# Performance work log

Hardware: AMD Instinct MI355X
Metric: run time of the kernel (lower is better)

The kernel has to match this reference:

```python
import jax, jax.numpy as jnp
import numpy as np


def setup_inputs() -> dict:
    key = jax.random.key(0)
    k1, k2 = jax.random.split(key)
    x = jax.random.normal(k1, (16, 8192, 128), dtype=jnp.float32)
    embed = jax.random.normal(k2, (1024, 128), dtype=jnp.float32)
    return {"x": x, "embed": embed}


def reference(x, embed):
    # preprocess: flatten leading dims -> (N, d)
    shape = x.shape
    xf = x.reshape(-1, shape[-1])  # (N, d)
    # quantize: negative squared Euclidean distance, argmax over codebook
    dist = (2.0 * (xf @ embed.T)
            - jnp.sum(xf * xf, axis=1, keepdims=True)
            - jnp.sum(embed * embed, axis=1)[None, :])
    embed_ind = jnp.argmax(dist, axis=-1)  # (N,)
    # postprocess indices back to input leading shape
    embed_ind = embed_ind.reshape(shape[:-1])
    # dequantize: embedding lookup
    quantize = embed[embed_ind]  # (..., d)
    return embed_ind, quantize
```

## Files before the change

kernel.cpp:

```cpp
#include <hip/hip_runtime.h>
#include <math.h>


typedef __attribute__((ext_vector_type(8)))  short short8_t;
typedef __attribute__((ext_vector_type(16))) float floatx16;

constexpr int D        = 128;
constexpr int KCODES   = 1024;
constexpr int NTILES   = 32;
constexpr int ROWS_BLK = 128;
constexpr float TAU    = 0.015f;

constexpr size_t WS_NCSQ = 0;
constexpr size_t WS_EHI  = 4096;
constexpr size_t WS_ELO  = WS_EHI + 262144;
constexpr size_t WS_EMBT = WS_ELO + 262144;

__device__ inline unsigned short bf16_rne(float v, float* back) {
    unsigned u = __float_as_uint(v);
    unsigned r = (u + 0x7FFFu + ((u >> 16) & 1u)) >> 16;
    *back = __uint_as_float(r << 16);
    return (unsigned short)r;
}

__global__ __launch_bounds__(256)
void ecb_prep(const float* __restrict__ embed, float* __restrict__ ncsq,
              unsigned short* __restrict__ ehi, unsigned short* __restrict__ elo,
              float* __restrict__ embT) {
    const int tid = threadIdx.x;
    const int cc = tid & 15;
    const int nl = tid >> 4;
    const int n  = blockIdx.x * 16 + nl;
    const int t = n >> 5, nn = n & 31;
    const float* src = embed + (size_t)n * D + cc * 8;
    float4 a = *(const float4*)src;
    float4 b = *(const float4*)(src + 4);
    float vv[8] = {a.x, a.y, a.z, a.w, b.x, b.y, b.z, b.w};
    float ss = 0.f;
    unsigned short hq[8], lq[8];
#pragma unroll
    for (int j = 0; j < 8; ++j) {
        ss = fmaf(vv[j], vv[j], ss);
        float hb, db;
        hq[j] = bf16_rne(vv[j], &hb);
        lq[j] = bf16_rne(vv[j] - hb, &db);
    }
    uint4 ph, pl;
    ph.x = (unsigned)hq[0] | ((unsigned)hq[1] << 16);
    ph.y = (unsigned)hq[2] | ((unsigned)hq[3] << 16);
    ph.z = (unsigned)hq[4] | ((unsigned)hq[5] << 16);
    ph.w = (unsigned)hq[6] | ((unsigned)hq[7] << 16);
    pl.x = (unsigned)lq[0] | ((unsigned)lq[1] << 16);
    pl.y = (unsigned)lq[2] | ((unsigned)lq[3] << 16);
    pl.z = (unsigned)lq[4] | ((unsigned)lq[5] << 16);
    pl.w = (unsigned)lq[6] | ((unsigned)lq[7] << 16);
    size_t dst = ((size_t)(t * 8 + (cc >> 1)) * 64 + (size_t)((cc & 1) * 32 + nn)) * 8;
    *(uint4*)(ehi + dst) = ph;
    *(uint4*)(elo + dst) = pl;
#pragma unroll
    for (int j = 0; j < 8; ++j) embT[(size_t)(cc * 8 + j) * KCODES + n] = vv[j];
#pragma unroll
    for (int m = 1; m < 16; m <<= 1) ss += __shfl_xor(ss, m, 64);
    if (cc == 0) ncsq[n] = -ss;
}

__global__ __launch_bounds__(256, 2)
void ecb_main(const float* __restrict__ x,
              const unsigned short* __restrict__ ehi, const unsigned short* __restrict__ elo,
              const float* __restrict__ ncsq, const float* __restrict__ embed,
              const float* __restrict__ embT,
              float* __restrict__ out_idx, float* __restrict__ out_q) {
    __shared__ int   sidx[ROWS_BLK];
    __shared__ unsigned char llist[ROWS_BLK];
    __shared__ unsigned lcount;
    __shared__ float xs[D];
    __shared__ float bv[256];
    __shared__ int   bi[256];

    const int tid  = threadIdx.x;
    const int lane = tid & 63, wave = tid >> 6;
    const int col  = lane & 31, h = lane >> 5;
    const long rowblk = (long)blockIdx.x * ROWS_BLK;
    const int  roww   = wave * 32;

    if (tid == 0) lcount = 0u;

    short8_t ah[8], al[8];
    {
        const float* xr = x + (rowblk + roww + col) * (long)D + h * 8;
#pragma unroll
        for (int c = 0; c < 8; ++c) {
            float4 a  = *(const float4*)(xr + c * 16);
            float4 b  = *(const float4*)(xr + c * 16 + 4);
            float vv[8] = {a.x, a.y, a.z, a.w, b.x, b.y, b.z, b.w};
            short8_t fh, fl;
#pragma unroll
            for (int j = 0; j < 8; ++j) {
                float v2x = vv[j] + vv[j];
                float hb, db;
                fh[j] = (short)bf16_rne(v2x, &hb);
                fl[j] = (short)bf16_rne(v2x - hb, &db);
            }
            ah[c] = fh;
            al[c] = fl;
        }
    }

    float v1[16], v2[16];
#pragma unroll
    for (int j = 0; j < 16; ++j) { v1[j] = -INFINITY; v2[j] = -INFINITY; }

    const short8_t* Bh = (const short8_t*)ehi + lane;
    const short8_t* Bl = (const short8_t*)elo + lane;

    __syncthreads();

#pragma unroll 1
    for (int t = 0; t < NTILES; ++t) {
        const float negcs = ncsq[t * 32 + col];
        short8_t bh[8], bl[8];
#pragma unroll
        for (int s = 0; s < 8; ++s) {
            bh[s] = Bh[(size_t)(t * 8 + s) * 64];
            bl[s] = Bl[(size_t)(t * 8 + s) * 64];
        }
        floatx16 accA, accB;
#pragma unroll
        for (int i = 0; i < 16; ++i) { accA[i] = negcs; accB[i] = 0.f; }
#pragma unroll
        for (int s = 0; s < 8; ++s) {
            accA = __builtin_amdgcn_mfma_f32_32x32x16_bf16(ah[s], bh[s], accA, 0, 0, 0);
            accB = __builtin_amdgcn_mfma_f32_32x32x16_bf16(al[s], bh[s], accB, 0, 0, 0);
            accB = __builtin_amdgcn_mfma_f32_32x32x16_bf16(ah[s], bl[s], accB, 0, 0, 0);
        }
#pragma unroll
        for (int j = 0; j < 16; ++j) {
            float sc = accA[j] + accB[j];
            unsigned u = (__float_as_uint(sc) & ~31u) | (unsigned)t;
            float cand = __uint_as_float(u);
            float mn = fminf(v1[j], cand);
            v1[j] = fmaxf(v1[j], cand);
            v2[j] = fmaxf(v2[j], mn);
        }
        __builtin_amdgcn_s_barrier();
    }

#pragma unroll
    for (int j = 0; j < 16; ++j) {
        float a1 = v1[j], a2 = v2[j];
        int   c1 = (int)((__float_as_uint(a1) & 31u) << 5) | col;
#pragma unroll
        for (int m = 1; m < 32; m <<= 1) {
            float o1 = __shfl_xor(a1, m, 64);
            int   oc = __shfl_xor(c1, m, 64);
            float o2 = __shfl_xor(a2, m, 64);
            float lo = fminf(a1, o1);
            if (o1 > a1) { a1 = o1; c1 = oc; }
            a2 = fmaxf(fmaxf(a2, o2), lo);
        }
        if (col == j) {
            int row_local = roww + (j & 3) + 8 * (j >> 2) + 4 * h;
            sidx[row_local] = c1;
            out_idx[rowblk + row_local] = (float)c1;
            if (a1 - a2 < TAU) {
                unsigned p = atomicAdd(&lcount, 1u);
                llist[p] = (unsigned char)row_local;
            }
        }
    }
    __syncthreads();

    for (int i = tid; i < ROWS_BLK * 32; i += 256) {
        int r = i >> 5, q = i & 31;
        int code = sidx[r];
        float4 ev = *(const float4*)(embed + (size_t)code * D + q * 4);
        *(float4*)(out_q + (rowblk + r) * (long)D + q * 4) = ev;
    }
    __syncthreads();

    const unsigned nf = lcount;
    const float4* eT = (const float4*)embT;
    for (unsigned f = 0; f < nf; ++f) {
        const int rl  = llist[f];
        const long row = rowblk + rl;
        if (tid < 32) *(float4*)&xs[tid * 4] = *(const float4*)(x + row * D + tid * 4);
        __syncthreads();
        float4 dot = {0.f, 0.f, 0.f, 0.f};
#pragma unroll 8
        for (int k = 0; k < D; ++k) {
            float xv = xs[k];
            float4 e = eT[(size_t)k * 256 + tid];
            dot.x = fmaf(xv, e.x, dot.x);
            dot.y = fmaf(xv, e.y, dot.y);
            dot.z = fmaf(xv, e.z, dot.z);
            dot.w = fmaf(xv, e.w, dot.w);
        }
        const int c0 = tid * 4;
        float scs[4] = {fmaf(2.f, dot.x, ncsq[c0]),
                        fmaf(2.f, dot.y, ncsq[c0 + 1]),
                        fmaf(2.f, dot.z, ncsq[c0 + 2]),
                        fmaf(2.f, dot.w, ncsq[c0 + 3])};
        float best = -INFINITY; int bidx = 0;
#pragma unroll
        for (int i = 0; i < 4; ++i)
            if (scs[i] > best) { best = scs[i]; bidx = c0 + i; }
        bv[tid] = best; bi[tid] = bidx;
        __syncthreads();
        for (int s = 128; s > 0; s >>= 1) {
            if (tid < s) {
                float ov = bv[tid + s]; int oi = bi[tid + s];
                if (ov > bv[tid] || (ov == bv[tid] && oi < bi[tid])) { bv[tid] = ov; bi[tid] = oi; }
            }
            __syncthreads();
        }
        const int win = bi[0];
        if (tid == 0) out_idx[row] = (float)win;
        if (tid < 32) {
            float4 ev = *(const float4*)(embed + (size_t)win * D + tid * 4);
            *(float4*)(out_q + row * D + tid * 4) = ev;
        }
        __syncthreads();
    }
}

extern "C" void kernel_launch(void* const* d_in, const int* in_sizes, int n_in,
                              void* d_out, int out_size, void* d_ws, size_t ws_size,
                              hipStream_t stream) {
    const float* x     = (const float*)d_in[0];
    const float* embed = (const float*)d_in[1];
    const int N = in_sizes[0] / D;
    char* ws = (char*)d_ws;
    float*          ncsq = (float*)(ws + WS_NCSQ);
    unsigned short* ehi  = (unsigned short*)(ws + WS_EHI);
    unsigned short* elo  = (unsigned short*)(ws + WS_ELO);
    float*          embT = (float*)(ws + WS_EMBT);
    float* out_idx = (float*)d_out;
    float* out_q   = out_idx + N;

    hipLaunchKernelGGL(ecb_prep, dim3(64), dim3(256), 0, stream,
                       embed, ncsq, ehi, elo, embT);
    hipLaunchKernelGGL(ecb_main, dim3(N / ROWS_BLK), dim3(256), 0, stream,
                       x, ehi, elo, ncsq, embed, embT, out_idx, out_q);
}
```

Baseline: 249.4 us.

## Double-buffer codebook tiles in LDS via async global_load_lds

Codebook bf16 hi/lo tiles are no longer loaded from global memory by every wave. Each tile is now staged once per block into a double-buffered LDS area with global_load_lds, so the next tile's load overlaps the current tile's MFMAs. ncsq is cached in shared memory, MFMA sections get raised wave priority, and launch bounds target 3 blocks per CU. The added waitcnt and barrier sync per tile and the tighter register budget may cost some of the gain.

```diff
diff --git a/kernel.cpp b/kernel.cpp
--- a/kernel.cpp
+++ b/kernel.cpp
@@ -15,6 +15,9 @@
 constexpr size_t WS_EHI  = 4096;
 constexpr size_t WS_ELO  = WS_EHI + 262144;
 constexpr size_t WS_EMBT = WS_ELO + 262144;
+
+#define GLOBAL_AS __attribute__((address_space(1)))
+#define LDS_AS    __attribute__((address_space(3)))
 
 __device__ inline unsigned short bf16_rne(float v, float* back) {
     unsigned u = __float_as_uint(v);
@@ -64,18 +67,17 @@
     if (cc == 0) ncsq[n] = -ss;
 }
 
-__global__ __launch_bounds__(256, 2)
+__global__ __launch_bounds__(256, 3)
 void ecb_main(const float* __restrict__ x,
               const unsigned short* __restrict__ ehi, const unsigned short* __restrict__ elo,
               const float* __restrict__ ncsq, const float* __restrict__ embed,
               const float* __restrict__ embT,
               float* __restrict__ out_idx, float* __restrict__ out_q) {
+    __shared__ short8_t ebuf[2][2][512];
+    __shared__ float ncsq_s[KCODES];
     __shared__ int   sidx[ROWS_BLK];
     __shared__ unsigned char llist[ROWS_BLK];
     __shared__ unsigned lcount;
-    __shared__ float xs[D];
-    __shared__ float bv[256];
-    __shared__ int   bi[256];
 
     const int tid  = threadIdx.x;
     const int lane = tid & 63, wave = tid >> 6;
@@ -84,6 +86,7 @@
     const int  roww   = wave * 32;
 
     if (tid == 0) lcount = 0u;
+    ((float4*)ncsq_s)[tid] = ((const float4*)ncsq)[tid];
 
     short8_t ah[8], al[8];
     {
@@ -106,33 +109,57 @@
         }
     }
 
+    auto stage = [&](int t, int bb) {
+        const char* gh = (const char*)ehi + (size_t)t * 8192;
+        const char* gl = (const char*)elo + (size_t)t * 8192;
+        char* lh = (char*)&ebuf[bb][0][0];
+        char* ll = (char*)&ebuf[bb][1][0];
+        const int off = wave * 2048;
+        __builtin_amdgcn_global_load_lds((const GLOBAL_AS unsigned int*)(gh + off + lane * 16),
+                                         (LDS_AS unsigned int*)(lh + off), 16, 0, 0);
+        __builtin_amdgcn_global_load_lds((const GLOBAL_AS unsigned int*)(gh + off + 1024 + lane * 16),
+                                         (LDS_AS unsigned int*)(lh + off + 1024), 16, 0, 0);
+        __builtin_amdgcn_global_load_lds((const GLOBAL_AS unsigned int*)(gl + off + lane * 16),
+                                         (LDS_AS unsigned int*)(ll + off), 16, 0, 0);
+        __builtin_amdgcn_global_load_lds((const GLOBAL_AS unsigned int*)(gl + off + 1024 + lane * 16),
+                                         (LDS_AS unsigned int*)(ll + off + 1024), 16, 0, 0);
+    };
+
     float v1[16], v2[16];
 #pragma unroll
     for (int j = 0; j < 16; ++j) { v1[j] = -INFINITY; v2[j] = -INFINITY; }
 
-    const short8_t* Bh = (const short8_t*)ehi + lane;
-    const short8_t* Bl = (const short8_t*)elo + lane;
-
     __syncthreads();
+    stage(0, 0);
 
 #pragma unroll 1
     for (int t = 0; t < NTILES; ++t) {
-        const float negcs = ncsq[t * 32 + col];
-        short8_t bh[8], bl[8];
+        const int b = t & 1;
+        if (t + 1 < NTILES) {
+            stage(t + 1, b ^ 1);
+            asm volatile("s_waitcnt vmcnt(4)" ::: "memory");
+        } else {
+            asm volatile("s_waitcnt vmcnt(0)" ::: "memory");
+        }
+        __builtin_amdgcn_sched_barrier(0);
+        __builtin_amdgcn_s_barrier();
+
+        const float negcs = ncsq_s[t * 32 + col];
+        floatx16 accA, accB;
+#pragma unroll
+        for (int i = 0; i < 16; ++i) { accA[i] = negcs; accB[i] = 0.f; }
+
+        __builtin_amdgcn_s_setprio(1);
 #pragma unroll
         for (int s = 0; s < 8; ++s) {
-            bh[s] = Bh[(size_t)(t * 8 + s) * 64];
-            bl[s] = Bl[(size_t)(t * 8 + s) * 64];
-        }
-        floatx16 accA, accB;
-#pragma unroll
-        for (int i = 0; i < 16; ++i) { accA[i] = negcs; accB[i] = 0.f; }
-#pragma unroll
-        for (int s = 0; s < 8; ++s) {
-            accA = __builtin_amdgcn_mfma_f32_32x32x16_bf16(ah[s], bh[s], accA, 0, 0, 0);
-            accB = __builtin_amdgcn_mfma_f32_32x32x16_bf16(al[s], bh[s], accB, 0, 0, 0);
-            accB = __builtin_amdgcn_mfma_f32_32x32x16_bf16(ah[s], bl[s], accB, 0, 0, 0);
-        }
+            short8_t bh = ebuf[b][0][s * 64 + lane];
+            short8_t bl = ebuf[b][1][s * 64 + lane];
+            accA = __builtin_amdgcn_mfma_f32_32x32x16_bf16(ah[s], bh, accA, 0, 0, 0);
+            accB = __builtin_amdgcn_mfma_f32_32x32x16_bf16(al[s], bh, accB, 0, 0, 0);
+            accB = __builtin_amdgcn_mfma_f32_32x32x16_bf16(ah[s], bl, accB, 0, 0, 0);
+        }
+        __builtin_amdgcn_s_setprio(0);
+
 #pragma unroll
         for (int j = 0; j < 16; ++j) {
             float sc = accA[j] + accB[j];
@@ -142,6 +169,9 @@
             v1[j] = fmaxf(v1[j], cand);
             v2[j] = fmaxf(v2[j], mn);
         }
+
+        asm volatile("s_waitcnt lgkmcnt(0)" ::: "memory");
+        __builtin_amdgcn_sched_barrier(0);
         __builtin_amdgcn_s_barrier();
     }
 
@@ -178,6 +208,9 @@
     }
     __syncthreads();
 
+    float* xs = (float*)&ebuf[0][0][0];
+    float* bv = xs + D;
+    int*   bi = (int*)(bv + 256);
     const unsigned nf = lcount;
     const float4* eT = (const float4*)embT;
     for (unsigned f = 0; f < nf; ++f) {
@@ -196,10 +229,10 @@
             dot.w = fmaf(xv, e.w, dot.w);
         }
         const int c0 = tid * 4;
-        float scs[4] = {fmaf(2.f, dot.x, ncsq[c0]),
-                        fmaf(2.f, dot.y, ncsq[c0 + 1]),
-                        fmaf(2.f, dot.z, ncsq[c0 + 2]),
-                        fmaf(2.f, dot.w, ncsq[c0 + 3])};
+        float scs[4] = {fmaf(2.f, dot.x, ncsq_s[c0]),
+                        fmaf(2.f, dot.y, ncsq_s[c0 + 1]),
+                        fmaf(2.f, dot.z, ncsq_s[c0 + 2]),
+                        fmaf(2.f, dot.w, ncsq_s[c0 + 3])};
         float best = -INFINITY; int bidx = 0;
 #pragma unroll
         for (int i = 0; i < 4; ++i)
```

Result: faster. 239.2 us (-4.1%).
